# Kernel tuning notes

Hardware: AMD Instinct MI355X
Metric: run time of the kernel (lower is better)

Reference implementation:

```python
import jax, jax.numpy as jnp
import numpy as np

B = 100000      # query points
L = 8           # num levels
N_RBF = 256     # RBF centers per level
F = 16          # features per level
OUT = 3         # output dim


def setup_inputs() -> dict:
    key = jax.random.key(0)
    k = jax.random.split(key, 6)
    x = jax.random.normal(k[0], (B, 3), dtype=jnp.float32)
    # small-magnitude features so gaussian RBF responses are non-degenerate
    feats = 0.1 * jax.random.normal(k[1], (B, L * F), dtype=jnp.float32)
    # centers initialized uniform(-1e-4, 1e-4) as in the torch module
    centers = jax.random.uniform(k[2], (L, N_RBF, F), dtype=jnp.float32,
                                 minval=-1e-4, maxval=1e-4)
    # log-width parameters (exp'd in forward); small perturbation around 0
    betas = 0.01 * jax.random.normal(k[3], (L, N_RBF, F), dtype=jnp.float32)
    W = jax.random.normal(k[4], (OUT, N_RBF * L), dtype=jnp.float32) / np.sqrt(N_RBF * L)
    b = jax.random.normal(k[5], (OUT,), dtype=jnp.float32) * 0.01
    return {"x": x, "feats": feats, "centers": centers, "betas": betas, "W": W, "b": b}


def reference(x, feats, centers, betas, W, b):
    # centers, betas: [L, N, F]. x is unused by the original forward (faithful).
    Lnum, N, f = centers.shape
    rbfs = []
    for i in range(Lnum):
        # concat of first i+1 per-level tables along feature axis -> [N, (i+1)*f]
        C = centers[: i + 1].transpose(1, 0, 2).reshape(N, (i + 1) * f)
        Bw = jnp.exp(betas[: i + 1].transpose(1, 0, 2).reshape(N, (i + 1) * f))
        x_in = feats[:, : (i + 1) * f]                      # [B, (i+1)*f]
        term1 = (x_in * x_in) @ Bw.T                        # [B, N]
        term2 = x_in @ (Bw * C).T                           # [B, N]
        term3 = jnp.sum(Bw * C * C, axis=1)                 # [N]
        dist_sq = term1 - 2.0 * term2 + term3[None, :]
        rbfs.append(jnp.exp(-0.5 * dist_sq))                # gaussian basis
    outs = jnp.concatenate(rbfs, axis=-1)                   # [B, L*N]
    return outs @ W.T + b
```

## Files before the change

kernel.cpp:

```cpp
#include <hip/hip_runtime.h>
#include <math.h>

#define LN 8
#define NRBF 256
#define FD 16
#define OUTD 3
#define KC (-0.72134752044f)

typedef __attribute__((ext_vector_type(8))) short short8;
typedef __attribute__((ext_vector_type(4))) float floatx4;
typedef __attribute__((ext_vector_type(2))) float floatx2;

__device__ __forceinline__ short f2bf(float f) {
    unsigned u = __builtin_bit_cast(unsigned, f);
    u += 0x7fffu + ((u >> 16) & 1u);
    return (short)(u >> 16);
}


__global__ __launch_bounds__(256) void prep(
    const float* __restrict__ centers, const float* __restrict__ betas,
    const float* __restrict__ W, short* __restrict__ PKB, float* __restrict__ EPI)
{
    __shared__ float ls[LN * 32];
    int blk = blockIdx.x;
    int tid = threadIdx.x;
    if (blk < 32) {
        int t = blk * 256 + tid;
        int lane = t & 63;
        int nt   = (t >> 6) & 15;
        int j    = t >> 10;
        int n    = nt * 16 + (lane & 15);
        int kq   = lane >> 4;
        size_t base = ((size_t)(j * NRBF + n)) * FD + kq * 4;
        float4 bq = *(const float4*)(betas + base);
        float4 cq = *(const float4*)(centers + base);
        float a0 = __expf(bq.x), a1 = __expf(bq.y), a2 = __expf(bq.z), a3 = __expf(bq.w);
        short8 v;
        v[0] = f2bf(a0); v[1] = f2bf(-2.0f * a0 * cq.x);
        v[2] = f2bf(a1); v[3] = f2bf(-2.0f * a1 * cq.y);
        v[4] = f2bf(a2); v[5] = f2bf(-2.0f * a2 * cq.z);
        v[6] = f2bf(a3); v[7] = f2bf(-2.0f * a3 * cq.w);
        *((short8*)(PKB + (size_t)t * 8)) = v;
    } else {
        int jj = tid >> 5;
        int nl = tid & 31;
        int n  = (blk - 32) * 32 + nl;
        const float* bp = betas   + ((size_t)(jj * NRBF + n)) * FD;
        const float* cp = centers + ((size_t)(jj * NRBF + n)) * FD;
        float s = 0.f;
#pragma unroll
        for (int q = 0; q < 4; ++q) {
            float4 bq = *(const float4*)(bp + q * 4);
            float4 cq = *(const float4*)(cp + q * 4);
            s = fmaf(__expf(bq.x) * cq.x, cq.x, s);
            s = fmaf(__expf(bq.y) * cq.y, cq.y, s);
            s = fmaf(__expf(bq.z) * cq.z, cq.z, s);
            s = fmaf(__expf(bq.w) * cq.w, cq.w, s);
        }
        ls[jj * 32 + nl] = s;
        __syncthreads();
        float t3 = 0.f;
        for (int j2 = 0; j2 <= jj; ++j2) t3 += ls[j2 * 32 + nl];
        float4 e;
        e.x = KC * t3;
        e.y = W[0 * (LN * NRBF) + jj * NRBF + n];
        e.z = W[1 * (LN * NRBF) + jj * NRBF + n];
        e.w = W[2 * (LN * NRBF) + jj * NRBF + n];
        int nt = n >> 4, l = n & 15;
        ((float4*)EPI)[nt * 128 + jj * 16 + l] = e;
    }
}

__global__ __launch_bounds__(256, 5) void rbf_mfma(
    const float* __restrict__ feats, const short* __restrict__ PKB,
    const float* __restrict__ EPI, const float* __restrict__ bias,
    float* __restrict__ out, int B)
{
    __shared__ float red[4][48];

    int tid  = threadIdx.x;
    int lane = tid & 63;
    int w    = tid >> 6;
    int b0   = blockIdx.x * 16;
    int m    = lane & 15;
    int kq   = lane >> 4;

    int brow = b0 + m; if (brow >= B) brow = B - 1;
    const float* xrow = feats + (size_t)brow * (LN * FD) + kq * 4;
    short8 afrag[LN];
#pragma unroll
    for (int j = 0; j < LN; ++j) {
        float4 x = *((const float4*)(xrow + j * FD));
        short8 f;
        f[0] = f2bf(x.x * x.x); f[1] = f2bf(x.x);
        f[2] = f2bf(x.y * x.y); f[3] = f2bf(x.y);
        f[4] = f2bf(x.z * x.z); f[5] = f2bf(x.z);
        f[6] = f2bf(x.w * x.w); f[7] = f2bf(x.w);
        afrag[j] = f;
    }

    floatx2 o01[4];
    float   o2[4];
#pragma unroll
    for (int r = 0; r < 4; ++r) { o01[r] = (floatx2){0.f, 0.f}; o2[r] = 0.f; }

#pragma unroll 1
    for (int g = 0; g < 4; ++g) {
        int nt = w * 4 + g;
        const short8* pb = (const short8*)PKB + (size_t)nt * 64 + lane;
        const float4* ep = (const float4*)EPI + (size_t)nt * 128 + m;
        floatx4 acc = {0.f, 0.f, 0.f, 0.f};
#pragma unroll
        for (int j = 0; j < LN; ++j) {
            short8 bfrag = pb[j * 16 * 64];
            float4 e     = ep[j * 16];
            acc = __builtin_amdgcn_mfma_f32_16x16x32_bf16(afrag[j], bfrag, acc, 0, 0, 0);
            floatx2 eyz = {e.y, e.z};
#pragma unroll
            for (int r = 0; r < 4; ++r) {
                float rv = __builtin_amdgcn_exp2f(fmaf(acc[r], KC, e.x));
                floatx2 rv2 = {rv, rv};
                o01[r] += rv2 * eyz;
                o2[r]   = fmaf(rv, e.w, o2[r]);
            }
        }
    }

    float oacc[12];
#pragma unroll
    for (int r = 0; r < 4; ++r) {
        oacc[r * 3 + 0] = o01[r].x;
        oacc[r * 3 + 1] = o01[r].y;
        oacc[r * 3 + 2] = o2[r];
    }
#pragma unroll
    for (int i = 0; i < 12; ++i) {
        oacc[i] += __shfl_xor(oacc[i], 1);
        oacc[i] += __shfl_xor(oacc[i], 2);
        oacc[i] += __shfl_xor(oacc[i], 4);
        oacc[i] += __shfl_xor(oacc[i], 8);
    }

    if (m < OUTD) {
#pragma unroll
        for (int r = 0; r < 4; ++r)
            red[w][kq * 12 + r * 3 + m] = oacc[r * 3 + m];
    }
    __syncthreads();

    if (tid < 48) {
        int o = tid % 3;
        int row = b0 + tid / 3;
        if (row < B) {
            float s = red[0][tid] + red[1][tid] + red[2][tid] + red[3][tid] + bias[o];
            out[(size_t)b0 * 3 + tid] = s;
        }
    }
}

extern "C" void kernel_launch(void* const* d_in, const int* in_sizes, int n_in,
                              void* d_out, int out_size, void* d_ws, size_t ws_size,
                              hipStream_t stream) {
    const float* feats   = (const float*)d_in[1];
    const float* centers = (const float*)d_in[2];
    const float* betas   = (const float*)d_in[3];
    const float* W       = (const float*)d_in[4];
    const float* bias    = (const float*)d_in[5];
    float* out = (float*)d_out;
    int B = in_sizes[1] / (LN * FD);

    short* PKB = (short*)d_ws;
    float* EPI = (float*)((char*)d_ws + 65536 * 2);

    prep<<<40, 256, 0, stream>>>(centers, betas, W, PKB, EPI);

    int tiles = (B + 15) / 16;
    rbf_mfma<<<tiles, 256, 0, stream>>>(feats, PKB, EPI, bias, out, B);
}
```

Baseline: 165.1 us.

## Give each wave its own 16-row tile and drop the cross-wave reduction

```diff
diff --git a/kernel.cpp b/kernel.cpp
--- a/kernel.cpp
+++ b/kernel.cpp
@@ -41,7 +41,7 @@
         v[2] = f2bf(a1); v[3] = f2bf(-2.0f * a1 * cq.y);
         v[4] = f2bf(a2); v[5] = f2bf(-2.0f * a2 * cq.z);
         v[6] = f2bf(a3); v[7] = f2bf(-2.0f * a3 * cq.w);
-        *((short8*)(PKB + (size_t)t * 8)) = v;
+        *((short8*)(PKB + (size_t)((nt * 8 + j) * 64 + lane) * 8)) = v;
     } else {
         int jj = tid >> 5;
         int nl = tid & 31;
@@ -72,19 +72,21 @@
     }
 }
 
-__global__ __launch_bounds__(256, 5) void rbf_mfma(
+__global__ __launch_bounds__(256, 4) void rbf_mfma(
     const float* __restrict__ feats, const short* __restrict__ PKB,
     const float* __restrict__ EPI, const float* __restrict__ bias,
     float* __restrict__ out, int B)
 {
-    __shared__ float red[4][48];
-
     int tid  = threadIdx.x;
     int lane = tid & 63;
-    int w    = tid >> 6;
-    int b0   = blockIdx.x * 16;
-    int m    = lane & 15;
-    int kq   = lane >> 4;
+    int wid  = tid >> 6;
+    int ntile_total = (B + 15) >> 4;
+    int tile = blockIdx.x * 4 + wid;
+    bool tvalid = (tile < ntile_total);
+    if (!tvalid) tile = ntile_total - 1;
+    int b0 = tile * 16;
+    int m  = lane & 15;
+    int kq = lane >> 4;
 
     int brow = b0 + m; if (brow >= B) brow = B - 1;
     const float* xrow = feats + (size_t)brow * (LN * FD) + kq * 4;
@@ -106,23 +108,33 @@
     for (int r = 0; r < 4; ++r) { o01[r] = (floatx2){0.f, 0.f}; o2[r] = 0.f; }
 
 #pragma unroll 1
-    for (int g = 0; g < 4; ++g) {
-        int nt = w * 4 + g;
-        const short8* pb = (const short8*)PKB + (size_t)nt * 64 + lane;
-        const float4* ep = (const float4*)EPI + (size_t)nt * 128 + m;
-        floatx4 acc = {0.f, 0.f, 0.f, 0.f};
+    for (int nt = 0; nt < 8; ++nt) {
+        const short8* pb0 = (const short8*)PKB + (size_t)(nt * 8) * 64 + lane;
+        const short8* pb1 = pb0 + (size_t)8 * 8 * 64;
+        const float4* ep0 = (const float4*)EPI + (size_t)nt * 128 + m;
+        const float4* ep1 = ep0 + (size_t)8 * 128;
+        floatx4 acc0 = {0.f, 0.f, 0.f, 0.f};
+        floatx4 acc1 = {0.f, 0.f, 0.f, 0.f};
 #pragma unroll
         for (int j = 0; j < LN; ++j) {
-            short8 bfrag = pb[j * 16 * 64];
-            float4 e     = ep[j * 16];
-            acc = __builtin_amdgcn_mfma_f32_16x16x32_bf16(afrag[j], bfrag, acc, 0, 0, 0);
-            floatx2 eyz = {e.y, e.z};
+            short8 bf0 = pb0[j * 64];
+            short8 bf1 = pb1[j * 64];
+            float4 e0  = ep0[j * 16];
+            float4 e1  = ep1[j * 16];
+            acc0 = __builtin_amdgcn_mfma_f32_16x16x32_bf16(afrag[j], bf0, acc0, 0, 0, 0);
+            acc1 = __builtin_amdgcn_mfma_f32_16x16x32_bf16(afrag[j], bf1, acc1, 0, 0, 0);
+            floatx2 eyz0 = {e0.y, e0.z};
+            floatx2 eyz1 = {e1.y, e1.z};
 #pragma unroll
             for (int r = 0; r < 4; ++r) {
-                float rv = __builtin_amdgcn_exp2f(fmaf(acc[r], KC, e.x));
-                floatx2 rv2 = {rv, rv};
-                o01[r] += rv2 * eyz;
-                o2[r]   = fmaf(rv, e.w, o2[r]);
+                float rv0 = __builtin_amdgcn_exp2f(fmaf(acc0[r], KC, e0.x));
+                float rv1 = __builtin_amdgcn_exp2f(fmaf(acc1[r], KC, e1.x));
+                floatx2 rv02 = {rv0, rv0};
+                floatx2 rv12 = {rv1, rv1};
+                o01[r] += rv02 * eyz0;
+                o01[r] += rv12 * eyz1;
+                o2[r]   = fmaf(rv0, e0.w, o2[r]);
+                o2[r]   = fmaf(rv1, e1.w, o2[r]);
             }
         }
     }
@@ -142,19 +154,12 @@
         oacc[i] += __shfl_xor(oacc[i], 8);
     }
 
-    if (m < OUTD) {
+    if (tvalid && m < OUTD) {
+        float bv = bias[m];
 #pragma unroll
-        for (int r = 0; r < 4; ++r)
-            red[w][kq * 12 + r * 3 + m] = oacc[r * 3 + m];
-    }
-    __syncthreads();
-
-    if (tid < 48) {
-        int o = tid % 3;
-        int row = b0 + tid / 3;
-        if (row < B) {
-            float s = red[0][tid] + red[1][tid] + red[2][tid] + red[3][tid] + bias[o];
-            out[(size_t)b0 * 3 + tid] = s;
+        for (int r = 0; r < 4; ++r) {
+            int row = b0 + kq * 4 + r;
+            if (row < B) out[(size_t)row * OUTD + m] = oacc[r * 3 + m] + bv;
         }
     }
 }
@@ -175,6 +180,7 @@
 
     prep<<<40, 256, 0, stream>>>(centers, betas, W, PKB, EPI);
 
-    int tiles = (B + 15) / 16;
-    rbf_mfma<<<tiles, 256, 0, stream>>>(feats, PKB, EPI, bias, out, B);
+    int tiles  = (B + 15) / 16;
+    int blocks = (tiles + 3) / 4;
+    rbf_mfma<<<blocks, 256, 0, stream>>>(feats, PKB, EPI, bias, out, B);
 }
```

Result: faster. 161.1 us (-2.4%).

## Reorder packed B fragments for contiguous per-tile loads and raise occupancy

Applied to the files above, without the earlier changes.

```diff
diff --git a/kernel.cpp b/kernel.cpp
--- a/kernel.cpp
+++ b/kernel.cpp
@@ -9,7 +9,6 @@
 
 typedef __attribute__((ext_vector_type(8))) short short8;
 typedef __attribute__((ext_vector_type(4))) float floatx4;
-typedef __attribute__((ext_vector_type(2))) float floatx2;
 
 __device__ __forceinline__ short f2bf(float f) {
     unsigned u = __builtin_bit_cast(unsigned, f);
@@ -41,7 +40,7 @@
         v[2] = f2bf(a1); v[3] = f2bf(-2.0f * a1 * cq.y);
         v[4] = f2bf(a2); v[5] = f2bf(-2.0f * a2 * cq.z);
         v[6] = f2bf(a3); v[7] = f2bf(-2.0f * a3 * cq.w);
-        *((short8*)(PKB + (size_t)t * 8)) = v;
+        *((short8*)(PKB + (size_t)((nt * 8 + j) * 64 + lane) * 8)) = v;
     } else {
         int jj = tid >> 5;
         int nl = tid & 31;
@@ -72,7 +71,7 @@
     }
 }
 
-__global__ __launch_bounds__(256, 5) void rbf_mfma(
+__global__ __launch_bounds__(256, 8) void rbf_mfma(
     const float* __restrict__ feats, const short* __restrict__ PKB,
     const float* __restrict__ EPI, const float* __restrict__ bias,
     float* __restrict__ out, int B)
@@ -81,7 +80,7 @@
 
     int tid  = threadIdx.x;
     int lane = tid & 63;
-    int w    = tid >> 6;
+    int w    = __builtin_amdgcn_readfirstlane(tid >> 6);
     int b0   = blockIdx.x * 16;
     int m    = lane & 15;
     int kq   = lane >> 4;
@@ -100,40 +99,31 @@
         afrag[j] = f;
     }
 
-    floatx2 o01[4];
-    float   o2[4];
+    float oacc[12];
 #pragma unroll
-    for (int r = 0; r < 4; ++r) { o01[r] = (floatx2){0.f, 0.f}; o2[r] = 0.f; }
+    for (int i = 0; i < 12; ++i) oacc[i] = 0.f;
 
 #pragma unroll 1
     for (int g = 0; g < 4; ++g) {
         int nt = w * 4 + g;
-        const short8* pb = (const short8*)PKB + (size_t)nt * 64 + lane;
+        const short8* pb = (const short8*)PKB + (size_t)(nt * 8) * 64 + lane;
         const float4* ep = (const float4*)EPI + (size_t)nt * 128 + m;
         floatx4 acc = {0.f, 0.f, 0.f, 0.f};
 #pragma unroll
         for (int j = 0; j < LN; ++j) {
-            short8 bfrag = pb[j * 16 * 64];
+            short8 bfrag = pb[j * 64];
             float4 e     = ep[j * 16];
             acc = __builtin_amdgcn_mfma_f32_16x16x32_bf16(afrag[j], bfrag, acc, 0, 0, 0);
-            floatx2 eyz = {e.y, e.z};
 #pragma unroll
             for (int r = 0; r < 4; ++r) {
                 float rv = __builtin_amdgcn_exp2f(fmaf(acc[r], KC, e.x));
-                floatx2 rv2 = {rv, rv};
-                o01[r] += rv2 * eyz;
-                o2[r]   = fmaf(rv, e.w, o2[r]);
+                oacc[r * 3 + 0] = fmaf(rv, e.y, oacc[r * 3 + 0]);
+                oacc[r * 3 + 1] = fmaf(rv, e.z, oacc[r * 3 + 1]);
+                oacc[r * 3 + 2] = fmaf(rv, e.w, oacc[r * 3 + 2]);
             }
         }
     }
 
-    float oacc[12];
-#pragma unroll
-    for (int r = 0; r < 4; ++r) {
-        oacc[r * 3 + 0] = o01[r].x;
-        oacc[r * 3 + 1] = o01[r].y;
-        oacc[r * 3 + 2] = o2[r];
-    }
 #pragma unroll
     for (int i = 0; i < 12; ++i) {
         oacc[i] += __shfl_xor(oacc[i], 1);
@@ -151,10 +141,10 @@
 
     if (tid < 48) {
         int o = tid % 3;
-        int row = b0 + tid / 3;
-        if (row < B) {
+        int idx = b0 * 3 + tid;
+        if (idx < B * 3) {
             float s = red[0][tid] + red[1][tid] + red[2][tid] + red[3][tid] + bias[o];
-            out[(size_t)b0 * 3 + tid] = s;
+            out[idx] = s;
         }
     }
 }
```

New measurement: 255.4 us. 54.7% more time.
